# Kernel optimization log

Measured on AMD Instinct MI355X. Metric: run time of the kernel, lower is better.

The kernel has to match this reference:

```python
import jax, jax.numpy as jnp
import numpy as np

N_LOCAL = 400
N_VOXEL = 200_000
N_EDGES = 1_200_000
D_LOCAL = 19
D_VOXEL = 6
NUM_CLASSES = 7
HIDDEN = 128
EPS = 1e-5  # GraphNorm eps


def _graph_norm(x, w, b, ms):
    # PyG GraphNorm with a single graph (batch=None): subtract scaled mean,
    # normalize by mean of squared centered values.
    mean = jnp.mean(x, axis=0, keepdims=True)
    out = x - ms * mean
    var = jnp.mean(out * out, axis=0, keepdims=True)
    return w * out * jax.lax.rsqrt(var + EPS) + b


def _gcn(x, src, dst, dinv, W, b, n):
    # GCNConv: symmetric-normalized aggregation with self-loops (already in src/dst)
    xw = x @ W
    msg = xw[src] * (dinv[src] * dinv[dst])[:, None]
    return jax.ops.segment_sum(msg, dst, num_segments=n) + b


def setup_inputs() -> dict:
    key = jax.random.key(0)
    ks = jax.random.split(key, 32)

    def p(k, shape, fan):
        return (jax.random.normal(k, shape, jnp.float32) / np.float32(np.sqrt(fan)))

    inp = {}
    inp["local_x"] = jax.random.normal(ks[0], (N_LOCAL, D_LOCAL), jnp.float32)
    inp["local_type"] = jax.random.randint(ks[1], (N_LOCAL,), 0, NUM_CLASSES)
    inp["voxel_x"] = jax.random.normal(ks[2], (N_VOXEL, D_VOXEL), jnp.float32)
    inp["voxel_type"] = jax.random.randint(ks[3], (N_VOXEL,), 0, NUM_CLASSES)
    inp["edge_index"] = jax.random.randint(ks[4], (2, N_EDGES), 0, N_VOXEL)
    inp["label_hard"] = jax.random.uniform(ks[5], (1, N_VOXEL, NUM_CLASSES), jnp.float32)

    din = D_LOCAL + D_VOXEL + NUM_CLASSES  # 32
    inp["We1"] = p(ks[6], (din, HIDDEN), din); inp["be1"] = jnp.zeros((HIDDEN,), jnp.float32)
    inp["We2"] = p(ks[7], (HIDDEN, HIDDEN), HIDDEN); inp["be2"] = jnp.zeros((HIDDEN,), jnp.float32)

    # encoder conv channels: 128->64->32->64->128 (REPEAT=2 down, then 2 up)
    conv_dims = [(128, 64), (64, 32), (32, 64), (64, 128)]
    for i, (a, b_) in enumerate(conv_dims):
        inp[f"Wc{i}"] = p(ks[8 + i], (a, b_), a)
        inp[f"bc{i}"] = jnp.zeros((b_,), jnp.float32)
        inp[f"gw{i}"] = jnp.ones((b_,), jnp.float32)
        inp[f"gb{i}"] = jnp.zeros((b_,), jnp.float32)
        inp[f"gm{i}"] = jnp.ones((b_,), jnp.float32)

    dec_dims = [(128, 64), (64, 32), (32, 16), (16, 1)]
    for i, (a, b_) in enumerate(dec_dims):
        inp[f"Wd{i}"] = p(ks[16 + i], (a, b_), a)
        inp[f"bd{i}"] = jnp.zeros((b_,), jnp.float32)
    return inp


def reference(local_x, local_type, voxel_x, voxel_type, edge_index, label_hard,
              We1, be1, We2, be2,
              Wc0, bc0, gw0, gb0, gm0,
              Wc1, bc1, gw1, gb1, gm1,
              Wc2, bc2, gw2, gb2, gm2,
              Wc3, bc3, gw3, gb3, gm3,
              Wd0, bd0, Wd1, bd1, Wd2, bd2, Wd3, bd3):
    n = voxel_x.shape[0]

    # --- masked type-match mean aggregation (vectorized segment mean) ---
    ones = jnp.ones((local_x.shape[0],), local_x.dtype)
    cnt = jax.ops.segment_sum(ones, local_type, num_segments=NUM_CLASSES)
    sums = jax.ops.segment_sum(local_x, local_type, num_segments=NUM_CLASSES)
    means = jnp.where(cnt[:, None] > 0, sums / jnp.maximum(cnt, 1.0)[:, None], 0.0)
    matched = means[voxel_type]  # [N_v, D_LOCAL]; zeros where type absent locally

    x = jnp.concatenate([matched, voxel_x, label_hard[0]], axis=-1)
    x = jax.nn.relu(x @ We1 + be1)
    x = jax.nn.relu(x @ We2 + be2)

    # --- GCN normalization with self-loops, computed once ---
    loop = jnp.arange(n)
    src = jnp.concatenate([edge_index[0], loop])
    dst = jnp.concatenate([edge_index[1], loop])
    deg = jax.ops.segment_sum(jnp.ones_like(dst, dtype=x.dtype), dst, num_segments=n)
    dinv = jax.lax.rsqrt(jnp.maximum(deg, 1.0))

    layers = [(Wc0, bc0, gw0, gb0, gm0), (Wc1, bc1, gw1, gb1, gm1),
              (Wc2, bc2, gw2, gb2, gm2), (Wc3, bc3, gw3, gb3, gm3)]
    for (W, b, gw, gb, gm) in layers:  # conv -> GraphNorm -> ReLU (Dropout = eval identity)
        x = _gcn(x, src, dst, dinv, W, b, n)
        x = jax.nn.relu(_graph_norm(x, gw, gb, gm))

    x = jax.nn.relu(x @ Wd0 + bd0)
    x = jax.nn.relu(x @ Wd1 + bd1)
    x = jax.nn.relu(x @ Wd2 + bd2)
    return jax.nn.sigmoid(x @ Wd3 + bd3)  # [N_v, 1]
```

## Files before the change

### kernel.cpp

```cpp
#include <hip/hip_runtime.h>
#include <hip/hip_bf16.h>
#include <cstddef>

#define THREADS 256
#define NSLOT 64

typedef unsigned short ushort_t;
typedef unsigned int uint_t;
typedef __attribute__((ext_vector_type(8))) short bf16x8;
typedef __attribute__((ext_vector_type(4))) float f32x4;

__device__ __forceinline__ ushort_t f2b(float f) {
    uint_t i = __float_as_uint(f);
    uint_t r = i + 0x7fffu + ((i >> 16) & 1u);
    return (ushort_t)(r >> 16);
}


__global__ __launch_bounds__(256) void local_means_kernel(const float* __restrict__ lx,
                                                          const int* __restrict__ lt,
                                                          float* __restrict__ means, int nl)
{
    __shared__ float slx[512 * 19];
    __shared__ int   slt[512];
    const int tid = threadIdx.x;
    for (int i = tid; i < nl * 19; i += 256) slx[i] = lx[i];
    for (int i = tid; i < nl; i += 256) slt[i] = lt[i];
    __syncthreads();
    if (tid >= 7 * 19) return;
    int c = tid / 19, dd = tid % 19;
    float s = 0.f; int cnt = 0;
    for (int i = 0; i < nl; ++i) {
        if (slt[i] == c) { s += slx[i * 19 + dd]; cnt++; }
    }
    means[tid] = cnt > 0 ? s / (float)cnt : 0.f;
}

__global__ void hist_kernel(const int* __restrict__ dst, int* __restrict__ degi, int E)
{
    int t = blockIdx.x * THREADS + threadIdx.x;
    if (t < E) atomicAdd(&degi[dst[t]], 1);
}

__global__ __launch_bounds__(256) void scan_part1_kernel(const int* __restrict__ degi,
                                                         int* __restrict__ blocksums, int n)
{
    const int tid = threadIdx.x;
    const int idx = blockIdx.x * 1024 + tid * 4;
    int v = 0;
    if (idx + 3 < n) {
        int4 d = *(const int4*)&degi[idx];
        v = d.x + d.y + d.z + d.w;
    } else {
        for (int i = 0; i < 4; ++i) if (idx + i < n) v += degi[idx + i];
    }
    __shared__ int s[256];
    s[tid] = v;
    __syncthreads();
    for (int off = 128; off >= 1; off >>= 1) {
        if (tid < off) s[tid] += s[tid + off];
        __syncthreads();
    }
    if (tid == 0) blocksums[blockIdx.x] = s[0];
}

__global__ __launch_bounds__(256) void scan_part2_kernel(int* __restrict__ blocksums, int nb)
{
    __shared__ int s[256];
    const int tid = threadIdx.x;
    int v = (tid < nb) ? blocksums[tid] : 0;
    s[tid] = v;
    __syncthreads();
    for (int off = 1; off < 256; off <<= 1) {
        int t = (tid >= off) ? s[tid - off] : 0;
        __syncthreads();
        s[tid] += t;
        __syncthreads();
    }
    if (tid < nb) blocksums[tid] = s[tid] - v;
}

__global__ __launch_bounds__(256) void scan_part3_kernel(const int* __restrict__ degi,
                                                         const int* __restrict__ blocksums,
                                                         int* __restrict__ rowptr,
                                                         int* __restrict__ cursor,
                                                         float* __restrict__ dinv, int n, int E)
{
    const int tid = threadIdx.x;
    const int idx = blockIdx.x * 1024 + tid * 4;
    int d0 = 0, d1 = 0, d2 = 0, d3 = 0;
    if (idx + 3 < n) {
        int4 d = *(const int4*)&degi[idx];
        d0 = d.x; d1 = d.y; d2 = d.z; d3 = d.w;
    } else {
        if (idx     < n) d0 = degi[idx];
        if (idx + 1 < n) d1 = degi[idx + 1];
        if (idx + 2 < n) d2 = degi[idx + 2];
        if (idx + 3 < n) d3 = degi[idx + 3];
    }
    const int v = d0 + d1 + d2 + d3;
    __shared__ int s[256];
    s[tid] = v;
    __syncthreads();
    for (int off = 1; off < 256; off <<= 1) {
        int t = (tid >= off) ? s[tid - off] : 0;
        __syncthreads();
        s[tid] += t;
        __syncthreads();
    }
    int run = blocksums[blockIdx.x] + s[tid] - v;
    if (idx + 3 < n) {
        int4 o;
        o.x = run; run += d0;
        o.y = run; run += d1;
        o.z = run; run += d2;
        o.w = run;
        *(int4*)&rowptr[idx] = o;
        *(int4*)&cursor[idx] = o;
        float4 dv;
        dv.x = rsqrtf((float)d0 + 1.0f);
        dv.y = rsqrtf((float)d1 + 1.0f);
        dv.z = rsqrtf((float)d2 + 1.0f);
        dv.w = rsqrtf((float)d3 + 1.0f);
        *(float4*)&dinv[idx] = dv;
    } else {
        if (idx     < n) { rowptr[idx]     = run; cursor[idx]     = run; dinv[idx]     = rsqrtf((float)d0 + 1.0f); run += d0; }
        if (idx + 1 < n) { rowptr[idx + 1] = run; cursor[idx + 1] = run; dinv[idx + 1] = rsqrtf((float)d1 + 1.0f); run += d1; }
        if (idx + 2 < n) { rowptr[idx + 2] = run; cursor[idx + 2] = run; dinv[idx + 2] = rsqrtf((float)d2 + 1.0f); run += d2; }
        if (idx + 3 < n) { rowptr[idx + 3] = run; cursor[idx + 3] = run; dinv[idx + 3] = rsqrtf((float)d3 + 1.0f); }
    }
    if (blockIdx.x == 0 && tid == 0) rowptr[n] = E;
}

__global__ void fill_kernel(const int* __restrict__ src, const int* __restrict__ dst,
                            int* __restrict__ cursor, int* __restrict__ esrc, int E)
{
    int t = blockIdx.x * THREADS + threadIdx.x;
    if (t >= E) return;
    int s = src[t], d = dst[t];
    int pos = atomicAdd(&cursor[d], 1);
    esrc[pos] = s;
}

__global__ void build_x0_kernel(const float* __restrict__ means,
                                const int* __restrict__ vt,
                                const float* __restrict__ vx,
                                const float* __restrict__ label,
                                float* __restrict__ out, int n)
{
    int tid = blockIdx.x * THREADS + threadIdx.x;
    int node = tid >> 5, c = tid & 31;
    if (node >= n) return;
    float v;
    if (c < 19)      v = means[vt[node] * 19 + c];
    else if (c < 25) v = vx[node * 6 + (c - 19)];
    else             v = label[node * 7 + (c - 25)];
    out[(size_t)node * 32 + c] = v;
}

__global__ void wtrans_kernel(const float* __restrict__ W, ushort_t* __restrict__ WT,
                              int din, int dout)
{
    int t = blockIdx.x * THREADS + threadIdx.x;
    if (t >= din * dout) return;
    int k = t / dout, c = t % dout;
    WT[(size_t)c * din + k] = f2b(W[t]);
}

template<int D>
__global__ void transform_kernel(const float* __restrict__ x, float* __restrict__ out,
                                 const float* __restrict__ tr, const float* __restrict__ dinv, int n)
{
    constexpr int Q = D / 4;
    int t = blockIdx.x * THREADS + threadIdx.x;
    int node = t / Q, q = t % Q;
    if (node >= n) return;
    float4 v = *(const float4*)&x[(size_t)node * D + q * 4];
    const float4 a = *(const float4*)&tr[q * 4];
    const float4 c = *(const float4*)&tr[D + q * 4];
    const float dd = dinv[node];
    float4 o;
    o.x = fmaxf(fmaf(v.x, a.x, c.x), 0.f) * dd;
    o.y = fmaxf(fmaf(v.y, a.y, c.y), 0.f) * dd;
    o.z = fmaxf(fmaf(v.z, a.z, c.z), 0.f) * dd;
    o.w = fmaxf(fmaf(v.w, a.w, c.w), 0.f) * dd;
    *(float4*)&out[(size_t)node * D + q * 4] = o;
}

template<int DIN, int DOUT, int BN, int JPER, bool RELU, bool BIAS, bool TRANSFORM, bool SCALE>
__global__ __launch_bounds__(256) void mlp_kernel(
    const float* __restrict__ in, float* __restrict__ out,
    const float* __restrict__ W, const float* __restrict__ bias,
    const float* __restrict__ tr, const float* __restrict__ rowscale, int n)
{
    constexpr int KT  = 32;
    constexpr int TJ  = DOUT / JPER;
    constexpr int TN  = 256 / TJ;
    constexpr int NPT = BN / TN;
    constexpr int JQ  = JPER / 4;
    constexpr int CS  = 4 * TJ;
    constexpr int BNP = BN + 4;

    __shared__ float Wt[KT * DOUT];
    __shared__ float xT[KT][BNP];

    const int tid   = threadIdx.x;
    const int nbase = blockIdx.x * BN;
    const int tj = tid % TJ, tn = tid / TJ;
    const int j0 = tj * 4, n0 = tn * NPT;

    float acc[NPT][JPER];
#pragma unroll
    for (int p = 0; p < NPT; ++p)
#pragma unroll
        for (int j = 0; j < JPER; ++j) acc[p][j] = 0.f;

    for (int kt = 0; kt < DIN; kt += KT) {
        __syncthreads();
        for (int i = tid * 4; i < KT * DOUT; i += THREADS * 4) {
            *(float4*)&Wt[i] = *(const float4*)&W[(size_t)kt * DOUT + i];
        }
        for (int i = tid; i < BN * (KT / 4); i += THREADS) {
            int node = i / (KT / 4);
            int kq   = i % (KT / 4);
            int g    = nbase + node;
            float4 v = make_float4(0.f, 0.f, 0.f, 0.f);
            if (g < n) {
                v = *(const float4*)&in[(size_t)g * DIN + kt + kq * 4];
                if (TRANSFORM) {
                    const float4 a = *(const float4*)&tr[kt + kq * 4];
                    const float4 c = *(const float4*)&tr[DIN + kt + kq * 4];
                    v.x = fmaxf(fmaf(v.x, a.x, c.x), 0.f);
                    v.y = fmaxf(fmaf(v.y, a.y, c.y), 0.f);
                    v.z = fmaxf(fmaf(v.z, a.z, c.z), 0.f);
                    v.w = fmaxf(fmaf(v.w, a.w, c.w), 0.f);
                }
            }
            xT[kq * 4 + 0][node] = v.x;
            xT[kq * 4 + 1][node] = v.y;
            xT[kq * 4 + 2][node] = v.z;
            xT[kq * 4 + 3][node] = v.w;
        }
        __syncthreads();
#pragma unroll 4
        for (int kk = 0; kk < KT; ++kk) {
            float wv[JPER];
#pragma unroll
            for (int q = 0; q < JQ; ++q)
                *(float4*)&wv[q * 4] = *(const float4*)&Wt[kk * DOUT + q * CS + j0];
            float xv[NPT];
#pragma unroll
            for (int q = 0; q < NPT / 4; ++q)
                *(float4*)&xv[q * 4] = *(const float4*)&xT[kk][n0 + q * 4];
#pragma unroll
            for (int p = 0; p < NPT; ++p)
#pragma unroll
                for (int j = 0; j < JPER; ++j)
                    acc[p][j] = fmaf(xv[p], wv[j], acc[p][j]);
        }
    }

    float bv[JPER];
#pragma unroll
    for (int j = 0; j < JPER; ++j) bv[j] = 0.f;
    if (BIAS) {
#pragma unroll
        for (int q = 0; q < JQ; ++q)
            *(float4*)&bv[q * 4] = *(const float4*)&bias[q * CS + j0];
    }

#pragma unroll
    for (int p = 0; p < NPT; ++p) {
        const int g = nbase + n0 + p;
        if (g >= n) continue;
        float rs = 1.f;
        if (SCALE) rs = rowscale[g];
#pragma unroll
        for (int q = 0; q < JQ; ++q) {
            float4 o;
            o.x = acc[p][q * 4 + 0] + bv[q * 4 + 0];
            o.y = acc[p][q * 4 + 1] + bv[q * 4 + 1];
            o.z = acc[p][q * 4 + 2] + bv[q * 4 + 2];
            o.w = acc[p][q * 4 + 3] + bv[q * 4 + 3];
            if (RELU) {
                o.x = fmaxf(o.x, 0.f); o.y = fmaxf(o.y, 0.f);
                o.z = fmaxf(o.z, 0.f); o.w = fmaxf(o.w, 0.f);
            }
            if (SCALE) { o.x *= rs; o.y *= rs; o.z *= rs; o.w *= rs; }
            *(float4*)&out[(size_t)g * DOUT + q * CS + j0] = o;
        }
    }
}

template<int DIN, int DOUT, bool RELU, bool BIAS, bool TRANSFORM, bool SCALE>
__global__ __launch_bounds__(256) void mfma_mlp_kernel(
    const float* __restrict__ in, float* __restrict__ out,
    const ushort_t* __restrict__ WT, const float* __restrict__ bias,
    const float* __restrict__ tr, const float* __restrict__ rowscale, int n)
{
    constexpr int BN  = 128;
    constexpr int KT  = 32;
    constexpr int NT  = DIN / KT;
    constexpr int LDK = 40;
    constexpr int WM  = 2, WN = 2;
    constexpr int MW  = BN / WM;
    constexpr int NW  = DOUT / WN;
    constexpr int MR  = MW / 16;
    constexpr int NR  = NW / 16;

    __shared__ ushort_t xA[BN * LDK];

    const int tid   = threadIdx.x;
    const int wid   = tid >> 6;
    const int lane  = tid & 63;
    const int wm    = wid >> 1, wn = wid & 1;
    const int nbase = blockIdx.x * BN;
    const int l16   = lane & 15;
    const int lk8   = (lane >> 4) * 8;

    f32x4 acc[MR][NR];
#pragma unroll
    for (int mi = 0; mi < MR; ++mi)
#pragma unroll
        for (int ni = 0; ni < NR; ++ni)
#pragma unroll
            for (int j = 0; j < 4; ++j) acc[mi][ni][j] = 0.f;

    for (int t = 0; t < NT; ++t) {
        const int kt = t * KT;
        __syncthreads();
        for (int i = tid; i < BN * (KT / 4); i += 256) {
            const int row = i / (KT / 4);
            const int kq  = (i % (KT / 4)) * 4;
            const int g   = nbase + row;
            float4 v = make_float4(0.f, 0.f, 0.f, 0.f);
            if (g < n) {
                v = *(const float4*)&in[(size_t)g * DIN + kt + kq];
                if (TRANSFORM) {
                    const float4 a = *(const float4*)&tr[kt + kq];
                    const float4 c = *(const float4*)&tr[DIN + kt + kq];
                    v.x = fmaxf(fmaf(v.x, a.x, c.x), 0.f);
                    v.y = fmaxf(fmaf(v.y, a.y, c.y), 0.f);
                    v.z = fmaxf(fmaf(v.z, a.z, c.z), 0.f);
                    v.w = fmaxf(fmaf(v.w, a.w, c.w), 0.f);
                }
            }
            ushort4 b;
            b.x = f2b(v.x); b.y = f2b(v.y); b.z = f2b(v.z); b.w = f2b(v.w);
            *(ushort4*)&xA[row * LDK + kq] = b;
        }
        __syncthreads();

        bf16x8 af[MR], bf[NR];
#pragma unroll
        for (int mi = 0; mi < MR; ++mi)
            af[mi] = *(const bf16x8*)&xA[(wm * MW + mi * 16 + l16) * LDK + lk8];
#pragma unroll
        for (int ni = 0; ni < NR; ++ni)
            bf[ni] = *(const bf16x8*)&WT[(size_t)(wn * NW + ni * 16 + l16) * DIN + kt + lk8];
#pragma unroll
        for (int mi = 0; mi < MR; ++mi)
#pragma unroll
            for (int ni = 0; ni < NR; ++ni)
                acc[mi][ni] = __builtin_amdgcn_mfma_f32_16x16x32_bf16(
                    af[mi], bf[ni], acc[mi][ni], 0, 0, 0);
    }

    float bv[NR];
#pragma unroll
    for (int ni = 0; ni < NR; ++ni)
        bv[ni] = BIAS ? bias[wn * NW + ni * 16 + l16] : 0.f;

#pragma unroll
    for (int mi = 0; mi < MR; ++mi) {
#pragma unroll
        for (int j = 0; j < 4; ++j) {
            const int r = wm * MW + mi * 16 + (lane >> 4) * 4 + j;
            const int g = nbase + r;
            if (g >= n) continue;
            float rs = 1.f;
            if (SCALE) rs = rowscale[g];
#pragma unroll
            for (int ni = 0; ni < NR; ++ni) {
                const int col = wn * NW + ni * 16 + l16;
                float v = acc[mi][ni][j] + bv[ni];
                if (RELU) v = fmaxf(v, 0.f);
                if (SCALE) v *= rs;
                out[(size_t)g * DOUT + col] = v;
            }
        }
    }
}

template<int D>
__global__ __launch_bounds__(256) void gather_agg_kernel(
    const float* __restrict__ y, float* __restrict__ out,
    const int* __restrict__ rowptr, const int* __restrict__ esrc,
    const float* __restrict__ dinv,
    const float* __restrict__ bias, float* __restrict__ statsP, int n)
{
    constexpr int JT  = D / 8;
    constexpr int NPB = 256 / JT;
    const int tid  = threadIdx.x;
    const int jq   = tid % JT;
    const int nsub = tid / JT;
    const int j0   = jq * 8;

    float bv[8];
#pragma unroll
    for (int e = 0; e < 8; ++e) bv[e] = bias[j0 + e];

    float s1[8], s2[8];
#pragma unroll
    for (int e = 0; e < 8; ++e) { s1[e] = 0.f; s2[e] = 0.f; }

    const int ntiles = (n + NPB - 1) / NPB;
    for (int tile = blockIdx.x; tile < ntiles; tile += gridDim.x) {
        const int node = tile * NPB + nsub;
        if (node < n) {
            const int rb = rowptr[node], re = rowptr[node + 1];
            const float dd = dinv[node];
            float acc[8];
            *(float4*)&acc[0] = *(const float4*)&y[(size_t)node * D + j0];
            *(float4*)&acc[4] = *(const float4*)&y[(size_t)node * D + j0 + 4];
            int k = rb;
            for (; k + 1 < re; k += 2) {
                const int sa = esrc[k], sb = esrc[k + 1];
                float4 a0 = *(const float4*)&y[(size_t)sa * D + j0];
                float4 a1 = *(const float4*)&y[(size_t)sa * D + j0 + 4];
                float4 b0 = *(const float4*)&y[(size_t)sb * D + j0];
                float4 b1 = *(const float4*)&y[(size_t)sb * D + j0 + 4];
                acc[0] += a0.x + b0.x; acc[1] += a0.y + b0.y;
                acc[2] += a0.z + b0.z; acc[3] += a0.w + b0.w;
                acc[4] += a1.x + b1.x; acc[5] += a1.y + b1.y;
                acc[6] += a1.z + b1.z; acc[7] += a1.w + b1.w;
            }
            if (k < re) {
                const int sa = esrc[k];
                float4 a0 = *(const float4*)&y[(size_t)sa * D + j0];
                float4 a1 = *(const float4*)&y[(size_t)sa * D + j0 + 4];
                acc[0] += a0.x; acc[1] += a0.y; acc[2] += a0.z; acc[3] += a0.w;
                acc[4] += a1.x; acc[5] += a1.y; acc[6] += a1.z; acc[7] += a1.w;
            }
            float o[8];
#pragma unroll
            for (int e = 0; e < 8; ++e) {
                o[e] = fmaf(acc[e], dd, bv[e]);
                s1[e] += o[e];
                s2[e] = fmaf(o[e], o[e], s2[e]);
            }
            *(float4*)&out[(size_t)node * D + j0]     = make_float4(o[0], o[1], o[2], o[3]);
            *(float4*)&out[(size_t)node * D + j0 + 4] = make_float4(o[4], o[5], o[6], o[7]);
        }
    }

    __shared__ float red[256][17];
#pragma unroll
    for (int e = 0; e < 8; ++e) { red[tid][e] = s1[e]; red[tid][8 + e] = s2[e]; }
    __syncthreads();
#pragma unroll
    for (int off = NPB / 2; off >= 1; off >>= 1) {
        if (nsub < off) {
#pragma unroll
            for (int e = 0; e < 16; ++e) red[tid][e] += red[tid + off * JT][e];
        }
        __syncthreads();
    }
    if (nsub == 0) {
        float* slot = statsP + (size_t)(blockIdx.x & (NSLOT - 1)) * 256;
#pragma unroll
        for (int e = 0; e < 8; ++e) {
            atomicAdd(&slot[j0 + e],     red[tid][e]);
            atomicAdd(&slot[D + j0 + e], red[tid][8 + e]);
        }
    }
}

template<int D>
__global__ __launch_bounds__(256) void gather_pre_kernel(
    const float* __restrict__ x, float* __restrict__ out,
    const int* __restrict__ rowptr, const int* __restrict__ esrc,
    const float* __restrict__ dinv, int n)
{
    constexpr int JT  = D / 8;
    constexpr int NPB = 256 / JT;
    const int tid  = threadIdx.x;
    const int jq   = tid % JT;
    const int nsub = tid / JT;
    const int j0   = jq * 8;

    const int ntiles = (n + NPB - 1) / NPB;
    for (int tile = blockIdx.x; tile < ntiles; tile += gridDim.x) {
        const int node = tile * NPB + nsub;
        if (node < n) {
            const int rb = rowptr[node], re = rowptr[node + 1];
            const float dd = dinv[node];
            float acc[8];
            *(float4*)&acc[0] = *(const float4*)&x[(size_t)node * D + j0];
            *(float4*)&acc[4] = *(const float4*)&x[(size_t)node * D + j0 + 4];
            int k = rb;
            for (; k + 1 < re; k += 2) {
                const int sa = esrc[k], sb = esrc[k + 1];
                float4 a0 = *(const float4*)&x[(size_t)sa * D + j0];
                float4 a1 = *(const float4*)&x[(size_t)sa * D + j0 + 4];
                float4 b0 = *(const float4*)&x[(size_t)sb * D + j0];
                float4 b1 = *(const float4*)&x[(size_t)sb * D + j0 + 4];
                acc[0] += a0.x + b0.x; acc[1] += a0.y + b0.y;
                acc[2] += a0.z + b0.z; acc[3] += a0.w + b0.w;
                acc[4] += a1.x + b1.x; acc[5] += a1.y + b1.y;
                acc[6] += a1.z + b1.z; acc[7] += a1.w + b1.w;
            }
            if (k < re) {
                const int sa = esrc[k];
                float4 a0 = *(const float4*)&x[(size_t)sa * D + j0];
                float4 a1 = *(const float4*)&x[(size_t)sa * D + j0 + 4];
                acc[0] += a0.x; acc[1] += a0.y; acc[2] += a0.z; acc[3] += a0.w;
                acc[4] += a1.x; acc[5] += a1.y; acc[6] += a1.z; acc[7] += a1.w;
            }
            float4 o0 = make_float4(acc[0] * dd, acc[1] * dd, acc[2] * dd, acc[3] * dd);
            float4 o1 = make_float4(acc[4] * dd, acc[5] * dd, acc[6] * dd, acc[7] * dd);
            *(float4*)&out[(size_t)node * D + j0]     = o0;
            *(float4*)&out[(size_t)node * D + j0 + 4] = o1;
        }
    }
}

template<int D>
__global__ __launch_bounds__(256) void gn_stats_kernel(const float* __restrict__ x,
                                                       float* __restrict__ statsP, int n)
{
    constexpr int JT   = D / 4;
    constexpr int NPB  = 256 / JT;
    constexpr int ITER = 32;
    const int tid  = threadIdx.x;
    const int jb   = tid % JT;
    const int rsub = tid / JT;
    const int j0   = jb * 4;
    const int base = blockIdx.x * NPB * ITER;

    float s1[4] = {0.f, 0.f, 0.f, 0.f};
    float s2[4] = {0.f, 0.f, 0.f, 0.f};

#pragma unroll 4
    for (int i = 0; i < ITER; ++i) {
        int r = base + rsub + i * NPB;
        if (r < n) {
            float4 v = *(const float4*)&x[(size_t)r * D + j0];
            s1[0] += v.x; s1[1] += v.y; s1[2] += v.z; s1[3] += v.w;
            s2[0] = fmaf(v.x, v.x, s2[0]);
            s2[1] = fmaf(v.y, v.y, s2[1]);
            s2[2] = fmaf(v.z, v.z, s2[2]);
            s2[3] = fmaf(v.w, v.w, s2[3]);
        }
    }

    __shared__ float red[256][9];
#pragma unroll
    for (int e = 0; e < 4; ++e) { red[tid][e] = s1[e]; red[tid][4 + e] = s2[e]; }
    __syncthreads();
#pragma unroll
    for (int off = NPB / 2; off >= 1; off >>= 1) {
        if (rsub < off) {
#pragma unroll
            for (int e = 0; e < 8; ++e) red[tid][e] += red[tid + off * JT][e];
        }
        __syncthreads();
    }
    if (rsub == 0) {
        float* slot = statsP + (size_t)(blockIdx.x & (NSLOT - 1)) * 256;
#pragma unroll
        for (int e = 0; e < 4; ++e) {
            atomicAdd(&slot[j0 + e],     red[tid][e]);
            atomicAdd(&slot[D + j0 + e], red[tid][4 + e]);
        }
    }
}

template<int D>
__global__ void gn_finalize_kernel(const float* __restrict__ part, float* __restrict__ ac,
                                   const float* __restrict__ gw, const float* __restrict__ gb,
                                   const float* __restrict__ gm, float inv_n)
{
    int j = threadIdx.x;
    if (j >= D) return;
    float s1 = 0.f, s2 = 0.f;
    for (int t = 0; t < NSLOT; ++t) {
        s1 += part[(size_t)t * 256 + j];
        s2 += part[(size_t)t * 256 + D + j];
    }
    float mean = s1 * inv_n;
    float ex2  = s2 * inv_n;
    float m    = gm[j];
    float var  = ex2 - (2.f * m - m * m) * mean * mean;
    float a    = gw[j] * rsqrtf(var + 1e-5f);
    float c    = gb[j] - a * m * mean;
    ac[j]     = a;
    ac[D + j] = c;
}

__global__ __launch_bounds__(256) void dec_tail_kernel(
    const float* __restrict__ in, const float* __restrict__ W1, const float* __restrict__ b1,
    const float* __restrict__ W2, const float* __restrict__ b2,
    const float* __restrict__ W3, const float* __restrict__ b3,
    float* __restrict__ out, int n)
{
    int t = blockIdx.x * THREADS + threadIdx.x;
    if (t >= n) return;

    float x[64];
#pragma unroll
    for (int q = 0; q < 16; ++q)
        *(float4*)&x[q * 4] = *(const float4*)&in[(size_t)t * 64 + q * 4];

    float h1[32];
#pragma unroll
    for (int j = 0; j < 32; ++j) h1[j] = b1[j];
#pragma unroll 8
    for (int k = 0; k < 64; ++k) {
        const float xk = x[k];
#pragma unroll
        for (int j = 0; j < 32; ++j) h1[j] = fmaf(xk, W1[k * 32 + j], h1[j]);
    }
#pragma unroll
    for (int j = 0; j < 32; ++j) h1[j] = fmaxf(h1[j], 0.f);

    float h2[16];
#pragma unroll
    for (int j = 0; j < 16; ++j) h2[j] = b2[j];
#pragma unroll 8
    for (int k = 0; k < 32; ++k) {
        const float hk = h1[k];
#pragma unroll
        for (int j = 0; j < 16; ++j) h2[j] = fmaf(hk, W2[k * 16 + j], h2[j]);
    }

    float acc = b3[0];
#pragma unroll
    for (int k = 0; k < 16; ++k) acc = fmaf(fmaxf(h2[k], 0.f), W3[k], acc);
    out[t] = 1.0f / (1.0f + expf(-acc));
}


extern "C" void kernel_launch(void* const* d_in, const int* in_sizes, int n_in,
                              void* d_out, int out_size, void* d_ws, size_t ws_size,
                              hipStream_t stream)
{
    const float* local_x    = (const float*)d_in[0];
    const int*   local_type = (const int*)d_in[1];
    const float* voxel_x    = (const float*)d_in[2];
    const int*   voxel_type = (const int*)d_in[3];
    const int*   edge_index = (const int*)d_in[4];
    const float* label      = (const float*)d_in[5];
    const float* We1 = (const float*)d_in[6],  *be1 = (const float*)d_in[7];
    const float* We2 = (const float*)d_in[8],  *be2 = (const float*)d_in[9];
    const float *Wc[4], *bc[4], *gw[4], *gb[4], *gm[4];
    for (int i = 0; i < 4; ++i) {
        Wc[i] = (const float*)d_in[10 + i * 5];
        bc[i] = (const float*)d_in[11 + i * 5];
        gw[i] = (const float*)d_in[12 + i * 5];
        gb[i] = (const float*)d_in[13 + i * 5];
        gm[i] = (const float*)d_in[14 + i * 5];
    }
    const float* Wd0 = (const float*)d_in[30], *bd0 = (const float*)d_in[31];
    const float* Wd1 = (const float*)d_in[32], *bd1 = (const float*)d_in[33];
    const float* Wd2 = (const float*)d_in[34], *bd2 = (const float*)d_in[35];
    const float* Wd3 = (const float*)d_in[36], *bd3 = (const float*)d_in[37];

    const int n  = in_sizes[2] / 6;
    const int E  = in_sizes[4] / 2;
    const int nl = in_sizes[0] / 19;
    const int* src = edge_index;
    const int* dst = edge_index + E;

    auto align256 = [](size_t x) { return (x + 255) & ~(size_t)255; };
    char* w = (char*)d_ws;
    float* ac_all = (float*)w;
    float* means  = (float*)(w + 4096);
    int* blocksums = (int*)(w + 8192);
    float* stats_part = (float*)(w + 8192 + 1024);
    size_t off = 8192 + 1024 + 4 * NSLOT * 256 * sizeof(float);
    ushort_t* wt0 = (ushort_t*)(w + off); off += align256(16384 * 2);
    ushort_t* wt1 = (ushort_t*)(w + off); off += align256(8192 * 2);
    ushort_t* wt2 = (ushort_t*)(w + off); off += align256(8192 * 2);
    ushort_t* wt3 = (ushort_t*)(w + off); off += align256(8192 * 2);
    int*   rowptr = (int*)(w + off);   off += align256((size_t)(n + 1) * 4);
    float* dinv   = (float*)(w + off); off += align256((size_t)n * 4);
    int*   esrc   = (int*)(w + off);   off += align256((size_t)E * 4);
    float* A    = (float*)(w + off);
    float* B    = A + (size_t)n * 128;
    float* A_lo = A;
    float* A_hi = A + (size_t)n * 64;
    float* B_lo = B;
    float* B_hi = B + (size_t)n * 64;
    int*   degi   = (int*)A;
    int*   cursor = (int*)A_hi;

    const float inv_n = 1.0f / (float)n;
    auto cdiv = [](long long a, long long b) { return (int)((a + b - 1) / b); };
    const int nb = cdiv(n, 1024);

    float* part0 = stats_part + 0 * NSLOT * 256;
    float* part1 = stats_part + 1 * NSLOT * 256;
    float* part2 = stats_part + 2 * NSLOT * 256;
    float* part3 = stats_part + 3 * NSLOT * 256;
    float* ac0 = ac_all + 0, *ac1 = ac_all + 256, *ac2 = ac_all + 512, *ac3 = ac_all + 768;

    hipMemsetAsync(stats_part, 0, 4 * NSLOT * 256 * sizeof(float), stream);
    hipMemsetAsync(degi, 0, (size_t)n * sizeof(int), stream);

    wtrans_kernel<<<cdiv(128 * 128, 256), 256, 0, stream>>>(We2,   wt0, 128, 128);
    wtrans_kernel<<<cdiv(128 * 64, 256), 256, 0, stream>>>(Wc[0], wt1, 128, 64);
    wtrans_kernel<<<cdiv(64 * 128, 256), 256, 0, stream>>>(Wc[3], wt2, 64, 128);
    wtrans_kernel<<<cdiv(128 * 64, 256), 256, 0, stream>>>(Wd0,   wt3, 128, 64);

    local_means_kernel<<<1, 256, 0, stream>>>(local_x, local_type, means, nl);
    hist_kernel<<<cdiv(E, 256), 256, 0, stream>>>(dst, degi, E);
    scan_part1_kernel<<<nb, 256, 0, stream>>>(degi, blocksums, n);
    scan_part2_kernel<<<1, 256, 0, stream>>>(blocksums, nb);
    scan_part3_kernel<<<nb, 256, 0, stream>>>(degi, blocksums, rowptr, cursor, dinv, n, E);
    fill_kernel<<<cdiv(E, 256), 256, 0, stream>>>(src, dst, cursor, esrc, E);
    build_x0_kernel<<<cdiv((long long)n * 32, 256), 256, 0, stream>>>(means, voxel_type, voxel_x, label, B_lo, n);

    const int gagg  = 2048;
    const int gmfma = cdiv(n, 128);

    mlp_kernel<32, 128, 128, 8, true, true, false, false><<<cdiv(n, 128), 256, 0, stream>>>(B_lo, A, We1, be1, nullptr, nullptr, n);
    mfma_mlp_kernel<128, 128, true, true, false, false><<<gmfma, 256, 0, stream>>>(A, B, wt0, be2, nullptr, nullptr, n);

    mfma_mlp_kernel<128, 64, false, false, false, true><<<gmfma, 256, 0, stream>>>(B, A_lo, wt1, nullptr, nullptr, dinv, n);
    gather_agg_kernel<64><<<gagg, 256, 0, stream>>>(A_lo, A_hi, rowptr, esrc, dinv, bc[0], part0, n);
    gn_finalize_kernel<64><<<1, 64, 0, stream>>>(part0, ac0, gw[0], gb[0], gm[0], inv_n);

    mlp_kernel<64, 32, 256, 4, false, false, true, true><<<cdiv(n, 256), 256, 0, stream>>>(A_hi, B_lo, Wc[1], nullptr, ac0, dinv, n);
    gather_agg_kernel<32><<<gagg, 256, 0, stream>>>(B_lo, B_hi, rowptr, esrc, dinv, bc[1], part1, n);
    gn_finalize_kernel<32><<<1, 32, 0, stream>>>(part1, ac1, gw[1], gb[1], gm[1], inv_n);

    transform_kernel<32><<<cdiv((long long)n * 8, 256), 256, 0, stream>>>(B_hi, B_lo, ac1, dinv, n);
    gather_pre_kernel<32><<<gagg, 256, 0, stream>>>(B_lo, A_lo, rowptr, esrc, dinv, n);
    mlp_kernel<32, 64, 256, 8, false, true, false, false><<<cdiv(n, 256), 256, 0, stream>>>(A_lo, B_hi, Wc[2], bc[2], nullptr, nullptr, n);
    gn_stats_kernel<64><<<cdiv(n, 512), 256, 0, stream>>>(B_hi, part2, n);
    gn_finalize_kernel<64><<<1, 64, 0, stream>>>(part2, ac2, gw[2], gb[2], gm[2], inv_n);

    transform_kernel<64><<<cdiv((long long)n * 16, 256), 256, 0, stream>>>(B_hi, A_lo, ac2, dinv, n);
    gather_pre_kernel<64><<<gagg, 256, 0, stream>>>(A_lo, B_lo, rowptr, esrc, dinv, n);
    mfma_mlp_kernel<64, 128, false, true, false, false><<<gmfma, 256, 0, stream>>>(B_lo, A, wt2, bc[3], nullptr, nullptr, n);
    gn_stats_kernel<128><<<cdiv(n, 256), 256, 0, stream>>>(A, part3, n);
    gn_finalize_kernel<128><<<1, 128, 0, stream>>>(part3, ac3, gw[3], gb[3], gm[3], inv_n);

    mfma_mlp_kernel<128, 64, true, true, true, false><<<gmfma, 256, 0, stream>>>(A, B_lo, wt3, bd0, ac3, nullptr, n);
    dec_tail_kernel<<<cdiv(n, 256), 256, 0, stream>>>(B_lo, Wd1, bd1, Wd2, bd2, Wd3, bd3, (float*)d_out, n);
}
```

Measured before the change: 730.1 us.

## Fuse GraphNorm transform into gather, record atomic slots in histogram, unroll gathers

Result: faster. 665.0 us (-8.9%).

```diff
diff --git a/kernel.cpp b/kernel.cpp
--- a/kernel.cpp
+++ b/kernel.cpp
@@ -36,10 +36,11 @@
     means[tid] = cnt > 0 ? s / (float)cnt : 0.f;
 }
 
-__global__ void hist_kernel(const int* __restrict__ dst, int* __restrict__ degi, int E)
+__global__ void hist_kernel(const int* __restrict__ dst, int* __restrict__ degi,
+                            int* __restrict__ qpos, int E)
 {
     int t = blockIdx.x * THREADS + threadIdx.x;
-    if (t < E) atomicAdd(&degi[dst[t]], 1);
+    if (t < E) qpos[t] = atomicAdd(&degi[dst[t]], 1);
 }
 
 __global__ __launch_bounds__(256) void scan_part1_kernel(const int* __restrict__ degi,
@@ -83,7 +84,6 @@
 __global__ __launch_bounds__(256) void scan_part3_kernel(const int* __restrict__ degi,
                                                          const int* __restrict__ blocksums,
                                                          int* __restrict__ rowptr,
-                                                         int* __restrict__ cursor,
                                                          float* __restrict__ dinv, int n, int E)
 {
     const int tid = threadIdx.x;
@@ -116,7 +116,6 @@
         o.z = run; run += d2;
         o.w = run;
         *(int4*)&rowptr[idx] = o;
-        *(int4*)&cursor[idx] = o;
         float4 dv;
         dv.x = rsqrtf((float)d0 + 1.0f);
         dv.y = rsqrtf((float)d1 + 1.0f);
@@ -124,22 +123,21 @@
         dv.w = rsqrtf((float)d3 + 1.0f);
         *(float4*)&dinv[idx] = dv;
     } else {
-        if (idx     < n) { rowptr[idx]     = run; cursor[idx]     = run; dinv[idx]     = rsqrtf((float)d0 + 1.0f); run += d0; }
-        if (idx + 1 < n) { rowptr[idx + 1] = run; cursor[idx + 1] = run; dinv[idx + 1] = rsqrtf((float)d1 + 1.0f); run += d1; }
-        if (idx + 2 < n) { rowptr[idx + 2] = run; cursor[idx + 2] = run; dinv[idx + 2] = rsqrtf((float)d2 + 1.0f); run += d2; }
-        if (idx + 3 < n) { rowptr[idx + 3] = run; cursor[idx + 3] = run; dinv[idx + 3] = rsqrtf((float)d3 + 1.0f); }
+        if (idx     < n) { rowptr[idx]     = run; dinv[idx]     = rsqrtf((float)d0 + 1.0f); run += d0; }
+        if (idx + 1 < n) { rowptr[idx + 1] = run; dinv[idx + 1] = rsqrtf((float)d1 + 1.0f); run += d1; }
+        if (idx + 2 < n) { rowptr[idx + 2] = run; dinv[idx + 2] = rsqrtf((float)d2 + 1.0f); run += d2; }
+        if (idx + 3 < n) { rowptr[idx + 3] = run; dinv[idx + 3] = rsqrtf((float)d3 + 1.0f); }
     }
     if (blockIdx.x == 0 && tid == 0) rowptr[n] = E;
 }
 
 __global__ void fill_kernel(const int* __restrict__ src, const int* __restrict__ dst,
-                            int* __restrict__ cursor, int* __restrict__ esrc, int E)
+                            const int* __restrict__ qpos, const int* __restrict__ rowptr,
+                            int* __restrict__ esrc, int E)
 {
     int t = blockIdx.x * THREADS + threadIdx.x;
     if (t >= E) return;
-    int s = src[t], d = dst[t];
-    int pos = atomicAdd(&cursor[d], 1);
-    esrc[pos] = s;
+    esrc[rowptr[dst[t]] + qpos[t]] = src[t];
 }
 
 __global__ void build_x0_kernel(const float* __restrict__ means,
@@ -165,26 +163,6 @@
     if (t >= din * dout) return;
     int k = t / dout, c = t % dout;
     WT[(size_t)c * din + k] = f2b(W[t]);
-}
-
-template<int D>
-__global__ void transform_kernel(const float* __restrict__ x, float* __restrict__ out,
-                                 const float* __restrict__ tr, const float* __restrict__ dinv, int n)
-{
-    constexpr int Q = D / 4;
-    int t = blockIdx.x * THREADS + threadIdx.x;
-    int node = t / Q, q = t % Q;
-    if (node >= n) return;
-    float4 v = *(const float4*)&x[(size_t)node * D + q * 4];
-    const float4 a = *(const float4*)&tr[q * 4];
-    const float4 c = *(const float4*)&tr[D + q * 4];
-    const float dd = dinv[node];
-    float4 o;
-    o.x = fmaxf(fmaf(v.x, a.x, c.x), 0.f) * dd;
-    o.y = fmaxf(fmaf(v.y, a.y, c.y), 0.f) * dd;
-    o.z = fmaxf(fmaf(v.z, a.z, c.z), 0.f) * dd;
-    o.w = fmaxf(fmaf(v.w, a.w, c.w), 0.f) * dd;
-    *(float4*)&out[(size_t)node * D + q * 4] = o;
 }
 
 template<int DIN, int DOUT, int BN, int JPER, bool RELU, bool BIAS, bool TRANSFORM, bool SCALE>
@@ -424,18 +402,27 @@
             *(float4*)&acc[0] = *(const float4*)&y[(size_t)node * D + j0];
             *(float4*)&acc[4] = *(const float4*)&y[(size_t)node * D + j0 + 4];
             int k = rb;
-            for (; k + 1 < re; k += 2) {
+            for (; k + 3 < re; k += 4) {
                 const int sa = esrc[k], sb = esrc[k + 1];
+                const int sc = esrc[k + 2], sd = esrc[k + 3];
                 float4 a0 = *(const float4*)&y[(size_t)sa * D + j0];
                 float4 a1 = *(const float4*)&y[(size_t)sa * D + j0 + 4];
                 float4 b0 = *(const float4*)&y[(size_t)sb * D + j0];
                 float4 b1 = *(const float4*)&y[(size_t)sb * D + j0 + 4];
-                acc[0] += a0.x + b0.x; acc[1] += a0.y + b0.y;
-                acc[2] += a0.z + b0.z; acc[3] += a0.w + b0.w;
-                acc[4] += a1.x + b1.x; acc[5] += a1.y + b1.y;
-                acc[6] += a1.z + b1.z; acc[7] += a1.w + b1.w;
-            }
-            if (k < re) {
+                float4 c0 = *(const float4*)&y[(size_t)sc * D + j0];
+                float4 c1 = *(const float4*)&y[(size_t)sc * D + j0 + 4];
+                float4 e0 = *(const float4*)&y[(size_t)sd * D + j0];
+                float4 e1 = *(const float4*)&y[(size_t)sd * D + j0 + 4];
+                acc[0] += (a0.x + b0.x) + (c0.x + e0.x);
+                acc[1] += (a0.y + b0.y) + (c0.y + e0.y);
+                acc[2] += (a0.z + b0.z) + (c0.z + e0.z);
+                acc[3] += (a0.w + b0.w) + (c0.w + e0.w);
+                acc[4] += (a1.x + b1.x) + (c1.x + e1.x);
+                acc[5] += (a1.y + b1.y) + (c1.y + e1.y);
+                acc[6] += (a1.z + b1.z) + (c1.z + e1.z);
+                acc[7] += (a1.w + b1.w) + (c1.w + e1.w);
+            }
+            for (; k < re; ++k) {
                 const int sa = esrc[k];
                 float4 a0 = *(const float4*)&y[(size_t)sa * D + j0];
                 float4 a1 = *(const float4*)&y[(size_t)sa * D + j0 + 4];
@@ -480,7 +467,7 @@
 __global__ __launch_bounds__(256) void gather_pre_kernel(
     const float* __restrict__ x, float* __restrict__ out,
     const int* __restrict__ rowptr, const int* __restrict__ esrc,
-    const float* __restrict__ dinv, int n)
+    const float* __restrict__ dinv, const float* __restrict__ tr, int n)
 {
     constexpr int JT  = D / 8;
     constexpr int NPB = 256 / JT;
@@ -489,33 +476,55 @@
     const int nsub = tid / JT;
     const int j0   = jq * 8;
 
+    float av[8], cv[8];
+#pragma unroll
+    for (int e = 0; e < 8; ++e) { av[e] = tr[j0 + e]; cv[e] = tr[D + j0 + e]; }
+
     const int ntiles = (n + NPB - 1) / NPB;
     for (int tile = blockIdx.x; tile < ntiles; tile += gridDim.x) {
         const int node = tile * NPB + nsub;
         if (node < n) {
             const int rb = rowptr[node], re = rowptr[node + 1];
             const float dd = dinv[node];
-            float acc[8];
-            *(float4*)&acc[0] = *(const float4*)&x[(size_t)node * D + j0];
-            *(float4*)&acc[4] = *(const float4*)&x[(size_t)node * D + j0 + 4];
+            float acc[8], v[8];
+            *(float4*)&v[0] = *(const float4*)&x[(size_t)node * D + j0];
+            *(float4*)&v[4] = *(const float4*)&x[(size_t)node * D + j0 + 4];
+#pragma unroll
+            for (int e = 0; e < 8; ++e)
+                acc[e] = fmaxf(fmaf(v[e], av[e], cv[e]), 0.f) * dd;
             int k = rb;
-            for (; k + 1 < re; k += 2) {
+            for (; k + 3 < re; k += 4) {
                 const int sa = esrc[k], sb = esrc[k + 1];
-                float4 a0 = *(const float4*)&x[(size_t)sa * D + j0];
-                float4 a1 = *(const float4*)&x[(size_t)sa * D + j0 + 4];
-                float4 b0 = *(const float4*)&x[(size_t)sb * D + j0];
-                float4 b1 = *(const float4*)&x[(size_t)sb * D + j0 + 4];
-                acc[0] += a0.x + b0.x; acc[1] += a0.y + b0.y;
-                acc[2] += a0.z + b0.z; acc[3] += a0.w + b0.w;
-                acc[4] += a1.x + b1.x; acc[5] += a1.y + b1.y;
-                acc[6] += a1.z + b1.z; acc[7] += a1.w + b1.w;
-            }
-            if (k < re) {
+                const int sc = esrc[k + 2], sd = esrc[k + 3];
+                const float da = dinv[sa], db = dinv[sb];
+                const float dc = dinv[sc], de = dinv[sd];
+                float va[8], vb[8], vc[8], ve[8];
+                *(float4*)&va[0] = *(const float4*)&x[(size_t)sa * D + j0];
+                *(float4*)&va[4] = *(const float4*)&x[(size_t)sa * D + j0 + 4];
+                *(float4*)&vb[0] = *(const float4*)&x[(size_t)sb * D + j0];
+                *(float4*)&vb[4] = *(const float4*)&x[(size_t)sb * D + j0 + 4];
+                *(float4*)&vc[0] = *(const float4*)&x[(size_t)sc * D + j0];
+                *(float4*)&vc[4] = *(const float4*)&x[(size_t)sc * D + j0 + 4];
+                *(float4*)&ve[0] = *(const float4*)&x[(size_t)sd * D + j0];
+                *(float4*)&ve[4] = *(const float4*)&x[(size_t)sd * D + j0 + 4];
+#pragma unroll
+                for (int e = 0; e < 8; ++e) {
+                    float fa = fmaxf(fmaf(va[e], av[e], cv[e]), 0.f) * da;
+                    float fb = fmaxf(fmaf(vb[e], av[e], cv[e]), 0.f) * db;
+                    float fc = fmaxf(fmaf(vc[e], av[e], cv[e]), 0.f) * dc;
+                    float fe = fmaxf(fmaf(ve[e], av[e], cv[e]), 0.f) * de;
+                    acc[e] += (fa + fb) + (fc + fe);
+                }
+            }
+            for (; k < re; ++k) {
                 const int sa = esrc[k];
-                float4 a0 = *(const float4*)&x[(size_t)sa * D + j0];
-                float4 a1 = *(const float4*)&x[(size_t)sa * D + j0 + 4];
-                acc[0] += a0.x; acc[1] += a0.y; acc[2] += a0.z; acc[3] += a0.w;
-                acc[4] += a1.x; acc[5] += a1.y; acc[6] += a1.z; acc[7] += a1.w;
+                const float da = dinv[sa];
+                float va[8];
+                *(float4*)&va[0] = *(const float4*)&x[(size_t)sa * D + j0];
+                *(float4*)&va[4] = *(const float4*)&x[(size_t)sa * D + j0 + 4];
+#pragma unroll
+                for (int e = 0; e < 8; ++e)
+                    acc[e] += fmaxf(fmaf(va[e], av[e], cv[e]), 0.f) * da;
             }
             float4 o0 = make_float4(acc[0] * dd, acc[1] * dd, acc[2] * dd, acc[3] * dd);
             float4 o1 = make_float4(acc[4] * dd, acc[5] * dd, acc[6] * dd, acc[7] * dd);
@@ -686,14 +695,14 @@
     int*   rowptr = (int*)(w + off);   off += align256((size_t)(n + 1) * 4);
     float* dinv   = (float*)(w + off); off += align256((size_t)n * 4);
     int*   esrc   = (int*)(w + off);   off += align256((size_t)E * 4);
+    int*   qpos   = (int*)(w + off);   off += align256((size_t)E * 4);
     float* A    = (float*)(w + off);
     float* B    = A + (size_t)n * 128;
     float* A_lo = A;
     float* A_hi = A + (size_t)n * 64;
     float* B_lo = B;
     float* B_hi = B + (size_t)n * 64;
-    int*   degi   = (int*)A;
-    int*   cursor = (int*)A_hi;
+    int*   degi = (int*)A;
 
     const float inv_n = 1.0f / (float)n;
     auto cdiv = [](long long a, long long b) { return (int)((a + b - 1) / b); };
@@ -714,11 +723,11 @@
     wtrans_kernel<<<cdiv(128 * 64, 256), 256, 0, stream>>>(Wd0,   wt3, 128, 64);
 
     local_means_kernel<<<1, 256, 0, stream>>>(local_x, local_type, means, nl);
-    hist_kernel<<<cdiv(E, 256), 256, 0, stream>>>(dst, degi, E);
+    hist_kernel<<<cdiv(E, 256), 256, 0, stream>>>(dst, degi, qpos, E);
     scan_part1_kernel<<<nb, 256, 0, stream>>>(degi, blocksums, n);
     scan_part2_kernel<<<1, 256, 0, stream>>>(blocksums, nb);
-    scan_part3_kernel<<<nb, 256, 0, stream>>>(degi, blocksums, rowptr, cursor, dinv, n, E);
-    fill_kernel<<<cdiv(E, 256), 256, 0, stream>>>(src, dst, cursor, esrc, E);
+    scan_part3_kernel<<<nb, 256, 0, stream>>>(degi, blocksums, rowptr, dinv, n, E);
+    fill_kernel<<<cdiv(E, 256), 256, 0, stream>>>(src, dst, qpos, rowptr, esrc, E);
     build_x0_kernel<<<cdiv((long long)n * 32, 256), 256, 0, stream>>>(means, voxel_type, voxel_x, label, B_lo, n);
 
     const int gagg  = 2048;
@@ -735,14 +744,12 @@
     gather_agg_kernel<32><<<gagg, 256, 0, stream>>>(B_lo, B_hi, rowptr, esrc, dinv, bc[1], part1, n);
     gn_finalize_kernel<32><<<1, 32, 0, stream>>>(part1, ac1, gw[1], gb[1], gm[1], inv_n);
 
-    transform_kernel<32><<<cdiv((long long)n * 8, 256), 256, 0, stream>>>(B_hi, B_lo, ac1, dinv, n);
-    gather_pre_kernel<32><<<gagg, 256, 0, stream>>>(B_lo, A_lo, rowptr, esrc, dinv, n);
+    gather_pre_kernel<32><<<gagg, 256, 0, stream>>>(B_hi, A_lo, rowptr, esrc, dinv, ac1, n);
     mlp_kernel<32, 64, 256, 8, false, true, false, false><<<cdiv(n, 256), 256, 0, stream>>>(A_lo, B_hi, Wc[2], bc[2], nullptr, nullptr, n);
     gn_stats_kernel<64><<<cdiv(n, 512), 256, 0, stream>>>(B_hi, part2, n);
     gn_finalize_kernel<64><<<1, 64, 0, stream>>>(part2, ac2, gw[2], gb[2], gm[2], inv_n);
 
-    transform_kernel<64><<<cdiv((long long)n * 16, 256), 256, 0, stream>>>(B_hi, A_lo, ac2, dinv, n);
-    gather_pre_kernel<64><<<gagg, 256, 0, stream>>>(A_lo, B_lo, rowptr, esrc, dinv, n);
+    gather_pre_kernel<64><<<gagg, 256, 0, stream>>>(B_hi, B_lo, rowptr, esrc, dinv, ac2, n);
     mfma_mlp_kernel<64, 128, false, true, false, false><<<gmfma, 256, 0, stream>>>(B_lo, A, wt2, bc[3], nullptr, nullptr, n);
     gn_stats_kernel<128><<<cdiv(n, 256), 256, 0, stream>>>(A, part3, n);
     gn_finalize_kernel<128><<<1, 128, 0, stream>>>(part3, ac3, gw[3], gb[3], gm[3], inv_n);
```
